# Kernel optimization log

Measured on AMD Instinct MI355X. Metric: run time of the kernel, lower is better.

The kernel has to match this reference:

```python
import jax, jax.numpy as jnp
import numpy as np

TEMPERATURE = 0.05
EPS = 1e-8  # torch.nn.CosineSimilarity eps


def setup_inputs() -> dict:
    key = jax.random.key(0)
    k1, k2 = jax.random.split(key)
    z1 = jax.random.normal(k1, (8192, 512), dtype=jnp.float32)
    z2 = jax.random.normal(k2, (8192, 512), dtype=jnp.float32)
    return {"z1": z1, "z2": z2}


def reference(z1, z2):
    # Pairwise cosine similarity via GEMM on raw dots / outer product of norms,
    # matching torch CosineSimilarity: dot / max(||a||*||b||, eps).
    dots = jnp.einsum('id,jd->ij', z1, z2)          # [N, N]
    n1 = jnp.linalg.norm(z1, axis=-1)               # [N]
    n2 = jnp.linalg.norm(z2, axis=-1)               # [N]
    denom = jnp.maximum(n1[:, None] * n2[None, :], EPS)
    sim = dots / denom / TEMPERATURE                # [N, N]
    return -jnp.mean(jax.scipy.special.logsumexp(sim, axis=-1))
```

## Files before the change

### kernel.cpp

```cpp
#include <hip/hip_runtime.h>
#include <hip/hip_fp8.h>

#define NROW 8192
#define DDIM 512
#define SCALE 20.0f
#define SHIFT 20.0f

#define BM 256
#define BN 256
#define BK 64
#define KT (DDIM / BK)
#define TILE_BYTES (BM * BK)
#define BUF_BYTES (2 * TILE_BYTES)
#define LDS_BYTES (2 * BUF_BYTES)

typedef __attribute__((ext_vector_type(4))) float f32x4;

__device__ __forceinline__ void gload16(const void* g, void* l) {
  __builtin_amdgcn_global_load_lds(
      (const __attribute__((address_space(1))) void*)g,
      (__attribute__((address_space(3))) void*)l,
      16, 0, 0);
}

__device__ __forceinline__ unsigned char to_e4m3(float x) {
  union { __hip_fp8_e4m3 f; unsigned char b; } u;
  u.f = __hip_fp8_e4m3(x);
  return u.b;
}

__global__ __launch_bounds__(256) void normalize_rows(
    const float* __restrict__ z1, const float* __restrict__ z2,
    unsigned char* __restrict__ z1n, unsigned char* __restrict__ z2n,
    float* __restrict__ rowsum) {
  int row = blockIdx.x * 4 + (threadIdx.x >> 6);
  int lane = threadIdx.x & 63;

  const float* src;
  unsigned char* dst;
  if (row < NROW) {
    src = z1 + (size_t)row * DDIM;
    dst = z1n + (size_t)row * DDIM;
    if (lane == 0) rowsum[row] = 0.0f;
  } else {
    int r = row - NROW;
    src = z2 + (size_t)r * DDIM;
    dst = z2n + (size_t)r * DDIM;
  }

  float4 v0 = *reinterpret_cast<const float4*>(src + lane * 8);
  float4 v1 = *reinterpret_cast<const float4*>(src + lane * 8 + 4);
  float ss = v0.x * v0.x + v0.y * v0.y + v0.z * v0.z + v0.w * v0.w +
             v1.x * v1.x + v1.y * v1.y + v1.z * v1.z + v1.w * v1.w;
#pragma unroll
  for (int off = 32; off; off >>= 1) ss += __shfl_xor(ss, off);

  float scale = SCALE / fmaxf(sqrtf(ss), 1e-8f);

  float vals[8] = {v0.x, v0.y, v0.z, v0.w, v1.x, v1.y, v1.z, v1.w};
  union { unsigned char b[8]; unsigned long long q; } pk;
#pragma unroll
  for (int j = 0; j < 8; ++j) pk.b[j] = to_e4m3(vals[j] * scale);
  *reinterpret_cast<unsigned long long*>(dst + lane * 8) = pk.q;
}

#define VMC(N) asm volatile("s_waitcnt vmcnt(" #N ")" ::: "memory")
#define SBAR()                          \
  do {                                  \
    __builtin_amdgcn_s_barrier();       \
    __builtin_amdgcn_sched_barrier(0);  \
  } while (0)

#define LDSA(BUFB, QM, MI, KK)                                                \
  (*reinterpret_cast<const long long*>(                                       \
      &ldsc[(size_t)(BUFB) * BUF_BYTES +                                      \
            (wr * 128 + (QM) * 64 + (MI) * 16 + l15) * 64 +                   \
            ((((KK) * 4 + hi) ^ e8) * 8)]))
#define LDSB(BUFB, QN, NI, KK)                                                \
  (*reinterpret_cast<const long long*>(                                       \
      &ldsc[(size_t)(BUFB) * BUF_BYTES + TILE_BYTES +                         \
            (wc * 64 + (QN) * 32 + (NI) * 16 + l15) * 64 +                    \
            ((((KK) * 4 + hi) ^ e8) * 8)]))

#define MF4(QM, MI, QN, BF)                                                   \
  acc[(QM) * 4 + (MI)][(QN) * 2 + 0] =                                        \
      __builtin_amdgcn_mfma_f32_16x16x32_fp8_fp8(                             \
          af[(MI) * 2 + 0], (BF)[0], acc[(QM) * 4 + (MI)][(QN) * 2 + 0],      \
          0, 0, 0);                                                           \
  acc[(QM) * 4 + (MI)][(QN) * 2 + 0] =                                        \
      __builtin_amdgcn_mfma_f32_16x16x32_fp8_fp8(                             \
          af[(MI) * 2 + 1], (BF)[1], acc[(QM) * 4 + (MI)][(QN) * 2 + 0],      \
          0, 0, 0);                                                           \
  acc[(QM) * 4 + (MI)][(QN) * 2 + 1] =                                        \
      __builtin_amdgcn_mfma_f32_16x16x32_fp8_fp8(                             \
          af[(MI) * 2 + 0], (BF)[2], acc[(QM) * 4 + (MI)][(QN) * 2 + 1],      \
          0, 0, 0);                                                           \
  acc[(QM) * 4 + (MI)][(QN) * 2 + 1] =                                        \
      __builtin_amdgcn_mfma_f32_16x16x32_fp8_fp8(                             \
          af[(MI) * 2 + 1], (BF)[3], acc[(QM) * 4 + (MI)][(QN) * 2 + 1],      \
          0, 0, 0);

#define PHASE_A(BUFB, QM, ST, H)                                              \
  do {                                                                        \
    af[0] = LDSA(BUFB, QM, 0, 0); af[1] = LDSA(BUFB, QM, 0, 1);               \
    af[2] = LDSA(BUFB, QM, 1, 0); af[3] = LDSA(BUFB, QM, 1, 1);               \
    STAGE_HALF(ST, H);                                                        \
    af[4] = LDSA(BUFB, QM, 2, 0); af[5] = LDSA(BUFB, QM, 2, 1);               \
    af[6] = LDSA(BUFB, QM, 3, 0); af[7] = LDSA(BUFB, QM, 3, 1);               \
    SBAR();                                                                   \
    __builtin_amdgcn_s_setprio(1);                                            \
    MF4(QM, 0, 0, bf0) MF4(QM, 1, 0, bf0)                                     \
    MF4(QM, 2, 0, bf0) MF4(QM, 3, 0, bf0)                                     \
    __builtin_amdgcn_s_setprio(0);                                            \
    SBAR();                                                                   \
  } while (0)

#define PHASE_B(BUFB, ST, H)                                                  \
  do {                                                                        \
    bf1[0] = LDSB(BUFB, 1, 0, 0); bf1[1] = LDSB(BUFB, 1, 0, 1);               \
    bf1[2] = LDSB(BUFB, 1, 1, 0); bf1[3] = LDSB(BUFB, 1, 1, 1);               \
    STAGE_HALF(ST, H);                                                        \
    SBAR();                                                                   \
    __builtin_amdgcn_s_setprio(1);                                            \
    MF4(0, 0, 1, bf1) MF4(0, 1, 1, bf1)                                       \
    MF4(0, 2, 1, bf1) MF4(0, 3, 1, bf1)                                       \
    __builtin_amdgcn_s_setprio(0);                                            \
    SBAR();                                                                   \
  } while (0)

#define PHASE_W(ST, PBUF)                                                     \
  do {                                                                        \
    STAGE_HALF(ST, 0);                                                        \
    VMC(1);                                                                   \
    SBAR();                                                                   \
    bf0[0] = LDSB(PBUF, 0, 0, 0); bf0[1] = LDSB(PBUF, 0, 0, 1);               \
    bf0[2] = LDSB(PBUF, 0, 1, 0); bf0[3] = LDSB(PBUF, 0, 1, 1);               \
    __builtin_amdgcn_s_setprio(1);                                            \
    MF4(1, 0, 1, bf1) MF4(1, 1, 1, bf1)                                       \
    MF4(1, 2, 1, bf1) MF4(1, 3, 1, bf1)                                       \
    __builtin_amdgcn_s_setprio(0);                                            \
    SBAR();                                                                   \
  } while (0)

__global__ __launch_bounds__(512, 2) void gemm_lse(
    const unsigned char* __restrict__ An,
    const unsigned char* __restrict__ Bn,
    float* __restrict__ rowsum) {
  extern __shared__ __align__(16) char ldsc[];

  const int bid = blockIdx.x;
  const int chunk = bid & 7;
  const int slot = bid >> 3;
  const int by = chunk * 4 + ((slot >> 2) & 3);
  const int bx = (slot >> 4) * 4 + (slot & 3);
  const int brow = by * BM;
  const int bcol = bx * BN;

  const int tid = threadIdx.x;
  const int w = tid >> 6;
  const int lane = tid & 63;
  const int wr = w >> 2;
  const int wc = w & 3;

  f32x4 acc[8][4];
#pragma unroll
  for (int m = 0; m < 8; ++m)
#pragma unroll
    for (int n = 0; n < 4; ++n) acc[m][n] = (f32x4)0.0f;

  const int srow = lane >> 2;
  const int spair = (lane & 3) ^ ((lane >> 3) & 3);

  auto STAGE_HALF = [&](int st, int h) {
    const int stm = st & (KT - 1);
    const unsigned char* gbase =
        (h < 2) ? An + (size_t)brow * DDIM : Bn + (size_t)bcol * DDIM;
    const int rowt = (h & 1) * 128 + w * 16;
    const unsigned char* g =
        gbase + (size_t)(rowt + srow) * DDIM + stm * BK + spair * 16;
    char* dst = ldsc + (size_t)(stm & 1) * BUF_BYTES +
                ((h >= 2) ? TILE_BYTES : 0) + rowt * 64;
    gload16(g, dst);
  };

  const int hi = lane >> 4;
  const int l15 = lane & 15;
  const int e8 = ((l15 >> 1) & 3) << 1;

  STAGE_HALF(0, 0); STAGE_HALF(0, 1); STAGE_HALF(0, 2); STAGE_HALF(0, 3);
  STAGE_HALF(1, 0);
  VMC(1);
  SBAR();

  long long af[8], bf0[4], bf1[4];
  bf0[0] = LDSB(0, 0, 0, 0); bf0[1] = LDSB(0, 0, 0, 1);
  bf0[2] = LDSB(0, 0, 1, 0); bf0[3] = LDSB(0, 0, 1, 1);

  for (int i = 0; i < KT / 2; ++i) {
    const int t1 = 2 * i + 1, t2 = 2 * i + 2, t3 = 2 * i + 3;
    PHASE_A(0, 0, t1, 1);
    PHASE_B(0, t1, 2);
    PHASE_A(0, 1, t1, 3);
    PHASE_W(t2, 1);
    PHASE_A(1, 0, t2, 1);
    PHASE_B(1, t2, 2);
    PHASE_A(1, 1, t2, 3);
    PHASE_W(t3, 0);
  }

  const float L2E20 = 1.4426950408889634f / 20.0f;
  const float NEG = -SHIFT * 1.4426950408889634f;
#pragma unroll
  for (int m = 0; m < 8; ++m) {
#pragma unroll
    for (int r = 0; r < 4; ++r) {
      float s = 0.0f;
#pragma unroll
      for (int n = 0; n < 4; ++n)
        s += exp2f(fmaf(acc[m][n][r], L2E20, NEG));
      s += __shfl_xor(s, 1);
      s += __shfl_xor(s, 2);
      s += __shfl_xor(s, 4);
      s += __shfl_xor(s, 8);
      if (l15 == 0)
        atomicAdd(&rowsum[brow + wr * 128 + m * 16 + hi * 4 + r], s);
    }
  }
}

__global__ __launch_bounds__(1024) void finalize_lse(
    const float* __restrict__ rowsum, float* __restrict__ out) {
  __shared__ float sm[16];
  float s = 0.0f;
  for (int i = threadIdx.x; i < NROW; i += 1024) s += logf(rowsum[i]);
#pragma unroll
  for (int off = 32; off; off >>= 1) s += __shfl_xor(s, off);
  int w = threadIdx.x >> 6;
  if ((threadIdx.x & 63) == 0) sm[w] = s;
  __syncthreads();
  if (threadIdx.x == 0) {
    float t = 0.0f;
#pragma unroll
    for (int i = 0; i < 16; ++i) t += sm[i];
    out[0] = -(t / (float)NROW + SHIFT);
  }
}

extern "C" void kernel_launch(void* const* d_in, const int* in_sizes, int n_in,
                              void* d_out, int out_size, void* d_ws,
                              size_t ws_size, hipStream_t stream) {
  const float* z1 = (const float*)d_in[0];
  const float* z2 = (const float*)d_in[1];
  float* out = (float*)d_out;

  char* ws = (char*)d_ws;
  unsigned char* z1n = (unsigned char*)ws;
  unsigned char* z2n = (unsigned char*)(ws + (size_t)NROW * DDIM);
  float* rowsum = (float*)(ws + (size_t)2 * NROW * DDIM);

  static bool attr_set = false;
  if (!attr_set) {
    hipFuncSetAttribute((const void*)gemm_lse,
                        hipFuncAttributeMaxDynamicSharedMemorySize, LDS_BYTES);
    attr_set = true;
  }

  normalize_rows<<<dim3((2 * NROW) / 4), dim3(256), 0, stream>>>(z1, z2, z1n,
                                                                 z2n, rowsum);
  gemm_lse<<<dim3((NROW / BM) * (NROW / BN)), dim3(512), LDS_BYTES, stream>>>(
      z1n, z2n, rowsum);
  finalize_lse<<<dim3(1), dim3(1024), 0, stream>>>(rowsum, out);
}
```

Baseline: 157.5 us.

## Replace phased half-tile ping-pong with 4-buffer ring prefetching two tiles ahead

```diff
diff --git a/kernel.cpp b/kernel.cpp
--- a/kernel.cpp
+++ b/kernel.cpp
@@ -12,7 +12,7 @@
 #define KT (DDIM / BK)
 #define TILE_BYTES (BM * BK)
 #define BUF_BYTES (2 * TILE_BYTES)
-#define LDS_BYTES (2 * BUF_BYTES)
+#define LDS_BYTES (4 * BUF_BYTES)
 
 typedef __attribute__((ext_vector_type(4))) float f32x4;
 
@@ -71,77 +71,6 @@
     __builtin_amdgcn_sched_barrier(0);  \
   } while (0)
 
-#define LDSA(BUFB, QM, MI, KK)                                                \
-  (*reinterpret_cast<const long long*>(                                       \
-      &ldsc[(size_t)(BUFB) * BUF_BYTES +                                      \
-            (wr * 128 + (QM) * 64 + (MI) * 16 + l15) * 64 +                   \
-            ((((KK) * 4 + hi) ^ e8) * 8)]))
-#define LDSB(BUFB, QN, NI, KK)                                                \
-  (*reinterpret_cast<const long long*>(                                       \
-      &ldsc[(size_t)(BUFB) * BUF_BYTES + TILE_BYTES +                         \
-            (wc * 64 + (QN) * 32 + (NI) * 16 + l15) * 64 +                    \
-            ((((KK) * 4 + hi) ^ e8) * 8)]))
-
-#define MF4(QM, MI, QN, BF)                                                   \
-  acc[(QM) * 4 + (MI)][(QN) * 2 + 0] =                                        \
-      __builtin_amdgcn_mfma_f32_16x16x32_fp8_fp8(                             \
-          af[(MI) * 2 + 0], (BF)[0], acc[(QM) * 4 + (MI)][(QN) * 2 + 0],      \
-          0, 0, 0);                                                           \
-  acc[(QM) * 4 + (MI)][(QN) * 2 + 0] =                                        \
-      __builtin_amdgcn_mfma_f32_16x16x32_fp8_fp8(                             \
-          af[(MI) * 2 + 1], (BF)[1], acc[(QM) * 4 + (MI)][(QN) * 2 + 0],      \
-          0, 0, 0);                                                           \
-  acc[(QM) * 4 + (MI)][(QN) * 2 + 1] =                                        \
-      __builtin_amdgcn_mfma_f32_16x16x32_fp8_fp8(                             \
-          af[(MI) * 2 + 0], (BF)[2], acc[(QM) * 4 + (MI)][(QN) * 2 + 1],      \
-          0, 0, 0);                                                           \
-  acc[(QM) * 4 + (MI)][(QN) * 2 + 1] =                                        \
-      __builtin_amdgcn_mfma_f32_16x16x32_fp8_fp8(                             \
-          af[(MI) * 2 + 1], (BF)[3], acc[(QM) * 4 + (MI)][(QN) * 2 + 1],      \
-          0, 0, 0);
-
-#define PHASE_A(BUFB, QM, ST, H)                                              \
-  do {                                                                        \
-    af[0] = LDSA(BUFB, QM, 0, 0); af[1] = LDSA(BUFB, QM, 0, 1);               \
-    af[2] = LDSA(BUFB, QM, 1, 0); af[3] = LDSA(BUFB, QM, 1, 1);               \
-    STAGE_HALF(ST, H);                                                        \
-    af[4] = LDSA(BUFB, QM, 2, 0); af[5] = LDSA(BUFB, QM, 2, 1);               \
-    af[6] = LDSA(BUFB, QM, 3, 0); af[7] = LDSA(BUFB, QM, 3, 1);               \
-    SBAR();                                                                   \
-    __builtin_amdgcn_s_setprio(1);                                            \
-    MF4(QM, 0, 0, bf0) MF4(QM, 1, 0, bf0)                                     \
-    MF4(QM, 2, 0, bf0) MF4(QM, 3, 0, bf0)                                     \
-    __builtin_amdgcn_s_setprio(0);                                            \
-    SBAR();                                                                   \
-  } while (0)
-
-#define PHASE_B(BUFB, ST, H)                                                  \
-  do {                                                                        \
-    bf1[0] = LDSB(BUFB, 1, 0, 0); bf1[1] = LDSB(BUFB, 1, 0, 1);               \
-    bf1[2] = LDSB(BUFB, 1, 1, 0); bf1[3] = LDSB(BUFB, 1, 1, 1);               \
-    STAGE_HALF(ST, H);                                                        \
-    SBAR();                                                                   \
-    __builtin_amdgcn_s_setprio(1);                                            \
-    MF4(0, 0, 1, bf1) MF4(0, 1, 1, bf1)                                       \
-    MF4(0, 2, 1, bf1) MF4(0, 3, 1, bf1)                                       \
-    __builtin_amdgcn_s_setprio(0);                                            \
-    SBAR();                                                                   \
-  } while (0)
-
-#define PHASE_W(ST, PBUF)                                                     \
-  do {                                                                        \
-    STAGE_HALF(ST, 0);                                                        \
-    VMC(1);                                                                   \
-    SBAR();                                                                   \
-    bf0[0] = LDSB(PBUF, 0, 0, 0); bf0[1] = LDSB(PBUF, 0, 0, 1);               \
-    bf0[2] = LDSB(PBUF, 0, 1, 0); bf0[3] = LDSB(PBUF, 0, 1, 1);               \
-    __builtin_amdgcn_s_setprio(1);                                            \
-    MF4(1, 0, 1, bf1) MF4(1, 1, 1, bf1)                                       \
-    MF4(1, 2, 1, bf1) MF4(1, 3, 1, bf1)                                       \
-    __builtin_amdgcn_s_setprio(0);                                            \
-    SBAR();                                                                   \
-  } while (0)
-
 __global__ __launch_bounds__(512, 2) void gemm_lse(
     const unsigned char* __restrict__ An,
     const unsigned char* __restrict__ Bn,
@@ -171,42 +100,86 @@
   const int srow = lane >> 2;
   const int spair = (lane & 3) ^ ((lane >> 3) & 3);
 
-  auto STAGE_HALF = [&](int st, int h) {
+  auto STAGE_TILE = [&](int st) {
     const int stm = st & (KT - 1);
-    const unsigned char* gbase =
-        (h < 2) ? An + (size_t)brow * DDIM : Bn + (size_t)bcol * DDIM;
-    const int rowt = (h & 1) * 128 + w * 16;
-    const unsigned char* g =
-        gbase + (size_t)(rowt + srow) * DDIM + stm * BK + spair * 16;
-    char* dst = ldsc + (size_t)(stm & 1) * BUF_BYTES +
-                ((h >= 2) ? TILE_BYTES : 0) + rowt * 64;
-    gload16(g, dst);
+    const int bo = (st & 3) * BUF_BYTES;
+#pragma unroll
+    for (int h = 0; h < 4; ++h) {
+      const unsigned char* gbase =
+          (h < 2) ? An + (size_t)brow * DDIM : Bn + (size_t)bcol * DDIM;
+      const int rowt = (h & 1) * 128 + w * 16;
+      const unsigned char* g =
+          gbase + (size_t)(rowt + srow) * DDIM + stm * BK + spair * 16;
+      char* dst = ldsc + bo + ((h >= 2) ? TILE_BYTES : 0) + rowt * 64;
+      gload16(g, dst);
+    }
   };
 
   const int hi = lane >> 4;
   const int l15 = lane & 15;
   const int e8 = ((l15 >> 1) & 3) << 1;
 
-  STAGE_HALF(0, 0); STAGE_HALF(0, 1); STAGE_HALF(0, 2); STAGE_HALF(0, 3);
-  STAGE_HALF(1, 0);
-  VMC(1);
+  const int paoff = (wr * 128 + l15) * 64;
+  const int pboff = TILE_BYTES + (wc * 64 + l15) * 64;
+  const int sa0 = ((0 + hi) ^ e8) * 8;
+  const int sa1 = ((4 + hi) ^ e8) * 8;
+
+  long long afr[16], bfr[8];
+
+  auto READF = [&](int bufb) {
+    const char* pa0 = ldsc + bufb * BUF_BYTES + paoff + sa0;
+    const char* pa1 = ldsc + bufb * BUF_BYTES + paoff + sa1;
+    const char* pb0 = ldsc + bufb * BUF_BYTES + pboff + sa0;
+    const char* pb1 = ldsc + bufb * BUF_BYTES + pboff + sa1;
+#pragma unroll
+    for (int qm = 0; qm < 2; ++qm)
+#pragma unroll
+      for (int mi = 0; mi < 4; ++mi) {
+        afr[qm * 8 + mi * 2 + 0] =
+            *(const long long*)(pa0 + (qm * 64 + mi * 16) * 64);
+        afr[qm * 8 + mi * 2 + 1] =
+            *(const long long*)(pa1 + (qm * 64 + mi * 16) * 64);
+      }
+#pragma unroll
+    for (int qn = 0; qn < 2; ++qn)
+#pragma unroll
+      for (int ni = 0; ni < 2; ++ni) {
+        bfr[qn * 4 + ni * 2 + 0] =
+            *(const long long*)(pb0 + (qn * 32 + ni * 16) * 64);
+        bfr[qn * 4 + ni * 2 + 1] =
+            *(const long long*)(pb1 + (qn * 32 + ni * 16) * 64);
+      }
+  };
+
+  STAGE_TILE(0);
+  STAGE_TILE(1);
+  VMC(4);
   SBAR();
 
-  long long af[8], bf0[4], bf1[4];
-  bf0[0] = LDSB(0, 0, 0, 0); bf0[1] = LDSB(0, 0, 0, 1);
-  bf0[2] = LDSB(0, 0, 1, 0); bf0[3] = LDSB(0, 0, 1, 1);
-
-  for (int i = 0; i < KT / 2; ++i) {
-    const int t1 = 2 * i + 1, t2 = 2 * i + 2, t3 = 2 * i + 3;
-    PHASE_A(0, 0, t1, 1);
-    PHASE_B(0, t1, 2);
-    PHASE_A(0, 1, t1, 3);
-    PHASE_W(t2, 1);
-    PHASE_A(1, 0, t2, 1);
-    PHASE_B(1, t2, 2);
-    PHASE_A(1, 1, t2, 3);
-    PHASE_W(t3, 0);
-  }
+#pragma unroll
+  for (int t = 0; t < KT; ++t) {
+    READF(t & 3);
+    STAGE_TILE(t + 2);
+    VMC(4);
+    SBAR();
+    __builtin_amdgcn_s_setprio(1);
+#pragma unroll
+    for (int kk = 0; kk < 2; ++kk)
+#pragma unroll
+      for (int qm = 0; qm < 2; ++qm)
+#pragma unroll
+        for (int mi = 0; mi < 4; ++mi)
+#pragma unroll
+          for (int qn = 0; qn < 2; ++qn)
+#pragma unroll
+            for (int ni = 0; ni < 2; ++ni)
+              acc[qm * 4 + mi][qn * 2 + ni] =
+                  __builtin_amdgcn_mfma_f32_16x16x32_fp8_fp8(
+                      afr[qm * 8 + mi * 2 + kk], bfr[qn * 4 + ni * 2 + kk],
+                      acc[qm * 4 + mi][qn * 2 + ni], 0, 0, 0);
+    __builtin_amdgcn_s_setprio(0);
+  }
+  VMC(0);
 
   const float L2E20 = 1.4426950408889634f / 20.0f;
   const float NEG = -SHIFT * 1.4426950408889634f;
```

New measurement: 153.4 us. 1.03x faster.
